# Optimization experiments

Measured on AMD Instinct MI355X. Metric: run time of the kernel, lower is better.

Reference implementation:

```python
import jax, jax.numpy as jnp
import numpy as np

IN_DIM = 256
QK_DIM = IN_DIM // 8


def setup_inputs() -> dict:
    key = jax.random.key(0)
    ks = jax.random.split(key, 10)
    B, C, W, H = 4, IN_DIM, 64, 64
    a = jax.random.normal(ks[0], (B, C, W, H), dtype=jnp.float32)
    b = jax.random.normal(ks[1], (B, C, W, H), dtype=jnp.float32)
    c = jax.random.uniform(ks[2], (B, 1, 2 * W, 2 * H), dtype=jnp.float32)
    scale = 0.02
    wq = jax.random.normal(ks[3], (QK_DIM, C), dtype=jnp.float32) * scale
    bq = jnp.zeros((QK_DIM,), dtype=jnp.float32)
    wk = jax.random.normal(ks[4], (QK_DIM, C), dtype=jnp.float32) * scale
    bk = jnp.zeros((QK_DIM,), dtype=jnp.float32)
    wv = jax.random.normal(ks[5], (C, C), dtype=jnp.float32) * scale
    bv = jnp.zeros((C,), dtype=jnp.float32)
    gamma = jnp.ones((1,), dtype=jnp.float32)
    return {"a": a, "b": b, "c": c, "wq": wq, "bq": bq, "wk": wk,
            "bk": bk, "wv": wv, "bv": bv, "gamma": gamma}


def reference(a, b, c, wq, bq, wk, bk, wv, bv, gamma):
    B, C, W, H = a.shape
    N = W * H
    # F.interpolate(c, scale_factor=1/down_rate, mode='nearest'): output idx i -> input idx i*down_rate
    down = c.shape[2] // W
    cd = c[:, :, ::down, ::down]                      # [B,1,W,H]
    # 1x1 convs as channel contractions
    q = jnp.einsum('bchw,oc->bohw', a, wq) + bq[None, :, None, None]
    k = jnp.einsum('bchw,oc->bohw', b, wk) + bk[None, :, None, None]
    v = jnp.einsum('bchw,oc->bohw', a, wv) + bv[None, :, None, None]
    qf = q.reshape(B, QK_DIM, N)                      # proj_query^T rows are spatial
    kf = k.reshape(B, QK_DIM, N)
    vf = v.reshape(B, C, N)
    sim = jnp.einsum('bdi,bdj->bij', qf, kf)          # [B,N,N]
    cflat = cd.reshape(B, N)
    # mask[b,i,j] = cflat[b,i] (per-query multiplicative logit scaling)
    logits = sim * cflat[:, :, None]
    attn = jax.nn.softmax(logits, axis=-1)            # [B,N,N]
    out_attn = jnp.einsum('bcj,bij->bci', vf, attn).reshape(B, C, W, H)
    out = gamma * a * cd + (1.0 - cd) * out_attn
    return out
```

## Files before the change

### kernel.cpp

```cpp
#include <hip/hip_runtime.h>

#define LOG2E 1.44269504088896340736f

typedef __attribute__((ext_vector_type(8))) short short8;
typedef __attribute__((ext_vector_type(4))) float float4v;
typedef __attribute__((ext_vector_type(2))) float float2v;
typedef __attribute__((ext_vector_type(2))) int int2v;
typedef __attribute__((ext_vector_type(4))) int int4v;

__device__ inline unsigned short f2bf(float f) {
    union { float f; unsigned u; } v; v.f = f;
    unsigned r = v.u + 0x7fffu + ((v.u >> 16) & 1u);
    return (unsigned short)(r >> 16);
}
__device__ inline float bf2f(unsigned short u) {
    union { unsigned u; float f; } v; v.u = ((unsigned)u) << 16;
    return v.f;
}
__device__ inline unsigned pk_bf16(float a, float b) {
    union { float f; unsigned u; } ua, ub; ua.f = a; ub.f = b;
    return __builtin_amdgcn_perm(ub.u + 0x8000u, ua.u + 0x8000u, 0x07060302u);
}

__global__ void wcvt_kernel(const float* __restrict__ wq, const float* __restrict__ wk,
                            const float* __restrict__ wv, unsigned short* __restrict__ Wbf)
{
    int idx = blockIdx.x * 256 + threadIdx.x;
    int e4  = idx * 4;
    int row = e4 >> 8, col = e4 & 255;
    const float* src = (row < 32) ? (wq + row * 256 + col)
                     : (row < 64) ? (wk + (row - 32) * 256 + col)
                                  : (wv + (row - 64) * 256 + col);
    float4v v = *(const float4v*)src;
    int2v p;
    p.x = (unsigned)f2bf(v[0]) | ((unsigned)f2bf(v[1]) << 16);
    p.y = (unsigned)f2bf(v[2]) | ((unsigned)f2bf(v[3]) << 16);
    *(int2v*)(Wbf + e4) = p;
}

__launch_bounds__(512, 2)
__global__ void proj_kernel(const float* __restrict__ a_p, const float* __restrict__ b_p,
                            const float* __restrict__ c_p,
                            const float* __restrict__ bq, const float* __restrict__ bk,
                            const float* __restrict__ bv,
                            const unsigned short* __restrict__ Wbf,
                            unsigned short* __restrict__ Qg, unsigned short* __restrict__ Kg,
                            unsigned short* __restrict__ Vg)
{
    __shared__ __align__(16) unsigned short At[64 * 264];
    __shared__ __align__(16) unsigned short Bt[64 * 264];
    __shared__ float bias[320];
    __shared__ float cdl[64];

    const int t    = threadIdx.x;
    const int blk  = blockIdx.x;
    const int b    = blk & 3;
    const int tile = blk >> 2;
    const int i0   = tile * 64;
    const int lane = t & 63;
    const int w    = t >> 6;
    const int q    = lane >> 4;
    const int n    = lane & 15;
    const int it   = w & 3;
    const int mh   = w >> 2;

    {
        const int arr = t >> 8, cp = (t >> 1) & 127, ih = (t & 1) * 32;
        const float* src = (arr ? b_p : a_p) + ((size_t)(b * 256 + 2 * cp)) * 4096 + i0 + ih;
        unsigned* dst = (unsigned*)(arr ? Bt : At) + cp;
#pragma unroll
        for (int h = 0; h < 4; ++h) {
            float4v r0a = *(const float4v*)(src + h * 8);
            float4v r0b = *(const float4v*)(src + h * 8 + 4);
            float4v r1a = *(const float4v*)(src + 4096 + h * 8);
            float4v r1b = *(const float4v*)(src + 4096 + h * 8 + 4);
#pragma unroll
            for (int jj = 0; jj < 4; ++jj)
                dst[(ih + h * 8 + jj) * 132] = pk_bf16(r0a[jj], r1a[jj]);
#pragma unroll
            for (int jj = 0; jj < 4; ++jj)
                dst[(ih + h * 8 + 4 + jj) * 132] = pk_bf16(r0b[jj], r1b[jj]);
        }
        if (t < 320) bias[t] = (t < 32) ? bq[t] : (t < 64) ? bk[t - 32] : bv[t - 64];
        else if (t < 384) cdl[t - 320] = c_p[b * 16384 + tile * 256 + (t - 320) * 2];
    }
    __syncthreads();

    float4v acc[10];
#pragma unroll
    for (int j = 0; j < 10; ++j) acc[j] = (float4v){0.f, 0.f, 0.f, 0.f};

#pragma unroll 2
    for (int kc = 0; kc < 8; ++kc) {
        short8 xa = *(const short8*)&At[(it * 16 + n) * 264 + kc * 32 + q * 8];
        short8 xb = xa;
        if (mh == 0)
            xb = *(const short8*)&Bt[(it * 16 + n) * 264 + kc * 32 + q * 8];
#pragma unroll
        for (int j = 0; j < 10; ++j) {
            int mt = mh * 10 + j;
            short8 wf = *(const short8*)(Wbf + (size_t)(mt * 16 + n) * 256 + kc * 32 + q * 8);
            short8 bsel = (mt == 2 || mt == 3) ? xb : xa;
            acc[j] = __builtin_amdgcn_mfma_f32_16x16x32_bf16(wf, bsel, acc[j], 0, 0, 0);
        }
    }
    __syncthreads();

    unsigned short* QKst = At;
    unsigned short* Vst  = Bt;
    {
        const float cdq = cdl[it * 16 + n] * LOG2E;
#pragma unroll
        for (int j = 0; j < 10; ++j) {
            int mt = mh * 10 + j;
            float4v bv4 = *(const float4v*)&bias[mt * 16 + q * 4];
            float v0 = acc[j][0] + bv4[0], v1 = acc[j][1] + bv4[1];
            float v2 = acc[j][2] + bv4[2], v3 = acc[j][3] + bv4[3];
            if (mt < 2) {
                v0 *= cdq; v1 *= cdq; v2 *= cdq; v3 *= cdq;
                int2v pk; pk.x = (int)pk_bf16(v0, v1); pk.y = (int)pk_bf16(v2, v3);
                *(int2v*)&QKst[(it * 16 + n) * 72 + mt * 16 + q * 4] = pk;
            } else if (mt < 4) {
                int2v pk; pk.x = (int)pk_bf16(v0, v1); pk.y = (int)pk_bf16(v2, v3);
                *(int2v*)&QKst[(it * 16 + n) * 72 + mt * 16 + q * 4] = pk;
            } else {
                int p = ((n >> 2) * 8) + ((it & 1) * 4) + (n & 3);
                int cbase = mt * 16 - 64 + q * 4;
                int jb = it >> 1;
                Vst[((jb * 256) + cbase + 0) * 32 + p] = f2bf(v0);
                Vst[((jb * 256) + cbase + 1) * 32 + p] = f2bf(v1);
                Vst[((jb * 256) + cbase + 2) * 32 + p] = f2bf(v2);
                Vst[((jb * 256) + cbase + 3) * 32 + p] = f2bf(v3);
            }
        }
    }
    __syncthreads();

    {
        int i = t >> 3, h8 = t & 7;
        int4v v = *(const int4v*)&QKst[i * 72 + h8 * 8];
        unsigned short* dstp = (h8 < 4)
            ? Qg + (size_t)(b * 4096 + i0 + i) * 32 + h8 * 8
            : Kg + (size_t)(b * 4096 + i0 + i) * 32 + (h8 - 4) * 8;
        *(int4v*)dstp = v;
    }
    {
#pragma unroll
        for (int k = 0; k < 4; ++k) {
            int flat = k * 512 + t;
            int4v v = *(const int4v*)&Vst[flat * 8];
            int jb = flat >> 10;
            *(int4v*)(Vg + (size_t)(b * 128 + tile * 2 + jb) * 8192 + (flat & 1023) * 8) = v;
        }
    }
}

__launch_bounds__(256, 3)
__global__ void attn_kernel(const unsigned short* __restrict__ Qg,
                            const unsigned short* __restrict__ Kg,
                            const unsigned short* __restrict__ Vg,
                            unsigned short* __restrict__ Opart, float* __restrict__ lsum)
{
    const int t    = threadIdx.x;
    const int blk  = blockIdx.x;
    const int b    = blk & 3;
    const int s_lo = (blk >> 2) & 1;
    const int rt   = (blk >> 3) & 63;
    const int s    = s_lo + 2 * (blk >> 9);
    const int lidx = (s << 8) | (rt << 2) | b;
    const int i0   = rt * 64;
    const int lane = t & 63;
    const int w    = t >> 6;
    const int q    = lane >> 4;
    const int n    = lane & 15;

    short8 qf[4];
#pragma unroll
    for (int ig = 0; ig < 4; ++ig)
        qf[ig] = *(const short8*)(Qg + (size_t)(b * 4096 + i0 + ig * 16 + n) * 32 + q * 8);

    float4v acc[4][4];
#pragma unroll
    for (int ig = 0; ig < 4; ++ig)
#pragma unroll
        for (int ct = 0; ct < 4; ++ct) acc[ig][ct] = (float4v){0.f, 0.f, 0.f, 0.f};
    float lsc[4] = {0.f, 0.f, 0.f, 0.f};

    const float4v m16v = (float4v){-16.f, -16.f, -16.f, -16.f};

    const unsigned short* kb = Kg + (size_t)(b * 4096 + s * 1024 + n) * 32 + q * 8;
    const unsigned short* vb = Vg + ((size_t)((b * 128 + s * 32) * 256 + w * 64 + n)) * 32 + q * 8;

    short8 kf0 = *(const short8*)(kb);
    short8 kf1 = *(const short8*)(kb + 512);

#pragma unroll 1
    for (int it = 0; it < 32; ++it) {
        short8 vf[4];
#pragma unroll
        for (int ct = 0; ct < 4; ++ct)
            vf[ct] = *(const short8*)(vb + ct * 512);

        short8 pf[4];
#pragma unroll
        for (int ig = 0; ig < 4; ++ig) {
            float4v s0 = __builtin_amdgcn_mfma_f32_16x16x32_bf16(kf0, qf[ig], m16v, 0, 0, 0);
            float4v s1 = __builtin_amdgcn_mfma_f32_16x16x32_bf16(kf1, qf[ig], m16v, 0, 0, 0);
            float p0 = __builtin_amdgcn_exp2f(s0[0]), p1 = __builtin_amdgcn_exp2f(s0[1]);
            float p2 = __builtin_amdgcn_exp2f(s0[2]), p3 = __builtin_amdgcn_exp2f(s0[3]);
            float p4 = __builtin_amdgcn_exp2f(s1[0]), p5 = __builtin_amdgcn_exp2f(s1[1]);
            float p6 = __builtin_amdgcn_exp2f(s1[2]), p7 = __builtin_amdgcn_exp2f(s1[3]);
            lsc[ig] += ((p0 + p1) + (p2 + p3)) + ((p4 + p5) + (p6 + p7));
            union { short8 s8; unsigned u[4]; } pf_;
            pf_.u[0] = pk_bf16(p0, p1);
            pf_.u[1] = pk_bf16(p2, p3);
            pf_.u[2] = pk_bf16(p4, p5);
            pf_.u[3] = pk_bf16(p6, p7);
            pf[ig] = pf_.s8;
        }

        kf0 = *(const short8*)(kb + 1024);
        kf1 = *(const short8*)(kb + 1536);

#pragma unroll
        for (int ig = 0; ig < 4; ++ig)
#pragma unroll
            for (int ct = 0; ct < 4; ++ct)
                acc[ig][ct] = __builtin_amdgcn_mfma_f32_16x16x32_bf16(pf[ig], vf[ct], acc[ig][ct], 0, 0, 0);

        kb += 1024;
        vb += 8192;
    }

    const size_t obase = (size_t)lidx * 16384;
#pragma unroll
    for (int ig = 0; ig < 4; ++ig)
#pragma unroll
        for (int ct = 0; ct < 4; ++ct) {
            int c = w * 64 + ct * 16 + n;
            int i = ig * 16 + q * 4;
            int2v pk;
            pk.x = (int)pk_bf16(acc[ig][ct][0], acc[ig][ct][1]);
            pk.y = (int)pk_bf16(acc[ig][ct][2], acc[ig][ct][3]);
            *(int2v*)(Opart + obase + (size_t)c * 64 + i) = pk;
        }
#pragma unroll
    for (int ig = 0; ig < 4; ++ig) {
        float v = lsc[ig];
        v += __shfl_xor(v, 16, 64);
        v += __shfl_xor(v, 32, 64);
        if (w == 0 && lane < 16)
            lsum[(size_t)lidx * 64 + ig * 16 + lane] = v;
    }
}

__launch_bounds__(256, 4)
__global__ void combine_kernel(const float* __restrict__ a_p, const float* __restrict__ c_p,
                               const float* __restrict__ gamma_p,
                               const unsigned short* __restrict__ Opart,
                               const float* __restrict__ lsum, float* __restrict__ out)
{
    __shared__ float invL[64];
    __shared__ float cdl[64];

    const int t   = threadIdx.x;
    const int blk = blockIdx.x;
    const int b   = blk & 3;
    const int rt  = (blk >> 2) & 63;
    const int cs  = blk >> 8;
    const int i0  = rt * 64;

    if (t < 64) {
        float L = 0.f;
#pragma unroll
        for (int s = 0; s < 4; ++s)
            L += lsum[(size_t)((s << 8) | (rt << 2) | b) * 64 + t];
        invL[t] = 1.0f / L;
        cdl[t] = c_p[b * 16384 + rt * 256 + 2 * t];
    }
    __syncthreads();

    const float gam = gamma_p[0];
    const int il = (t & 31) * 2;
    const int cq = t >> 5;
#pragma unroll
    for (int k = 0; k < 4; ++k) {
        int c = cs * 32 + cq + 8 * k;
        float o0 = 0.f, o1 = 0.f;
#pragma unroll
        for (int s = 0; s < 4; ++s) {
            int idx = (s << 8) | (rt << 2) | b;
            unsigned pr = *(const unsigned*)(Opart + (size_t)idx * 16384 + (size_t)c * 64 + il);
            o0 += bf2f((unsigned short)(pr & 0xffff));
            o1 += bf2f((unsigned short)(pr >> 16));
        }
        o0 *= invL[il];
        o1 *= invL[il + 1];
        size_t gi = (size_t)(b * 256 + c) * 4096 + i0 + il;
        float2v av = *(const float2v*)(a_p + gi);
        float cd0 = cdl[il], cd1 = cdl[il + 1];
        float2v ov;
        ov[0] = gam * av[0] * cd0 + (1.0f - cd0) * o0;
        ov[1] = gam * av[1] * cd1 + (1.0f - cd1) * o1;
        *(float2v*)(out + gi) = ov;
    }
}

extern "C" void kernel_launch(void* const* d_in, const int* in_sizes, int n_in,
                              void* d_out, int out_size, void* d_ws, size_t ws_size,
                              hipStream_t stream)
{
    const float* a_p   = (const float*)d_in[0];
    const float* b_p   = (const float*)d_in[1];
    const float* c_p   = (const float*)d_in[2];
    const float* wq    = (const float*)d_in[3];
    const float* bq    = (const float*)d_in[4];
    const float* wk    = (const float*)d_in[5];
    const float* bk    = (const float*)d_in[6];
    const float* wv    = (const float*)d_in[7];
    const float* bv    = (const float*)d_in[8];
    const float* gamma = (const float*)d_in[9];
    float* out = (float*)d_out;

    unsigned short* Qg    = (unsigned short*)d_ws;
    unsigned short* Kg    = Qg + (size_t)4 * 4096 * 32;
    unsigned short* Vg    = Kg + (size_t)4 * 4096 * 32;
    unsigned short* Wbf   = Vg + (size_t)4 * 256 * 4096;
    unsigned short* Opart = Wbf + (size_t)320 * 256;
    float*          lsum  = (float*)(Opart + (size_t)1024 * 16384);

    wcvt_kernel<<<80, 256, 0, stream>>>(wq, wk, wv, Wbf);
    proj_kernel<<<256, 512, 0, stream>>>(a_p, b_p, c_p, bq, bk, bv, Wbf, Qg, Kg, Vg);
    attn_kernel<<<1024, 256, 0, stream>>>(Qg, Kg, Vg, Opart, lsum);
    combine_kernel<<<2048, 256, 0, stream>>>(a_p, c_p, gamma, Opart, lsum, out);
}
```

Before: 188.4 us.

## Fuse weight bf16 conversion into projection, re-layout staging, add MFMA priority

Removes the separate weight-conversion kernel so the projection kernel reads fp32 weights and packs them to bf16 in registers right before each MFMA, saving one launch and a workspace round-trip. The activation staging loop is restructured so consecutive threads load consecutive pixels, and the LDS row stride is changed to 133 words to avoid bank conflicts. The attention kernel raises wave priority around the P·V MFMA block. The cost is that each of the 256 projection blocks now reads fp32 weights and converts them redundantly, which doubles weight load bytes and adds ALU work in the inner loop.

```diff
diff --git a/kernel.cpp b/kernel.cpp
--- a/kernel.cpp
+++ b/kernel.cpp
@@ -22,33 +22,18 @@
     return __builtin_amdgcn_perm(ub.u + 0x8000u, ua.u + 0x8000u, 0x07060302u);
 }
 
-__global__ void wcvt_kernel(const float* __restrict__ wq, const float* __restrict__ wk,
-                            const float* __restrict__ wv, unsigned short* __restrict__ Wbf)
-{
-    int idx = blockIdx.x * 256 + threadIdx.x;
-    int e4  = idx * 4;
-    int row = e4 >> 8, col = e4 & 255;
-    const float* src = (row < 32) ? (wq + row * 256 + col)
-                     : (row < 64) ? (wk + (row - 32) * 256 + col)
-                                  : (wv + (row - 64) * 256 + col);
-    float4v v = *(const float4v*)src;
-    int2v p;
-    p.x = (unsigned)f2bf(v[0]) | ((unsigned)f2bf(v[1]) << 16);
-    p.y = (unsigned)f2bf(v[2]) | ((unsigned)f2bf(v[3]) << 16);
-    *(int2v*)(Wbf + e4) = p;
-}
-
 __launch_bounds__(512, 2)
 __global__ void proj_kernel(const float* __restrict__ a_p, const float* __restrict__ b_p,
                             const float* __restrict__ c_p,
+                            const float* __restrict__ wq_p, const float* __restrict__ wk_p,
+                            const float* __restrict__ wv_p,
                             const float* __restrict__ bq, const float* __restrict__ bk,
                             const float* __restrict__ bv,
-                            const unsigned short* __restrict__ Wbf,
                             unsigned short* __restrict__ Qg, unsigned short* __restrict__ Kg,
                             unsigned short* __restrict__ Vg)
 {
-    __shared__ __align__(16) unsigned short At[64 * 264];
-    __shared__ __align__(16) unsigned short Bt[64 * 264];
+    __shared__ __align__(16) unsigned short At[64 * 266];
+    __shared__ __align__(16) unsigned short Bt[64 * 266];
     __shared__ float bias[320];
     __shared__ float cdl[64];
 
@@ -65,21 +50,19 @@
     const int mh   = w >> 2;
 
     {
-        const int arr = t >> 8, cp = (t >> 1) & 127, ih = (t & 1) * 32;
-        const float* src = (arr ? b_p : a_p) + ((size_t)(b * 256 + 2 * cp)) * 4096 + i0 + ih;
-        unsigned* dst = (unsigned*)(arr ? Bt : At) + cp;
-#pragma unroll
-        for (int h = 0; h < 4; ++h) {
-            float4v r0a = *(const float4v*)(src + h * 8);
-            float4v r0b = *(const float4v*)(src + h * 8 + 4);
-            float4v r1a = *(const float4v*)(src + 4096 + h * 8);
-            float4v r1b = *(const float4v*)(src + 4096 + h * 8 + 4);
-#pragma unroll
-            for (int jj = 0; jj < 4; ++jj)
-                dst[(ih + h * 8 + jj) * 132] = pk_bf16(r0a[jj], r1a[jj]);
-#pragma unroll
-            for (int jj = 0; jj < 4; ++jj)
-                dst[(ih + h * 8 + 4 + jj) * 132] = pk_bf16(r0b[jj], r1b[jj]);
+        const int arr = t >> 8, tt = t & 255;
+        unsigned* dst = (unsigned*)(arr ? Bt : At);
+        const float* base = (arr ? b_p : a_p) + (size_t)b * 256 * 4096 + i0;
+#pragma unroll
+        for (int r = 0; r < 8; ++r) {
+            int task = r * 256 + tt;
+            int cp = task >> 4, px4 = (task & 15) * 4;
+            const float* s0 = base + (size_t)(2 * cp) * 4096 + px4;
+            float4v r0 = *(const float4v*)s0;
+            float4v r1 = *(const float4v*)(s0 + 4096);
+#pragma unroll
+            for (int k = 0; k < 4; ++k)
+                dst[(px4 + k) * 133 + cp] = pk_bf16(r0[k], r1[k]);
         }
         if (t < 320) bias[t] = (t < 32) ? bq[t] : (t < 64) ? bk[t - 32] : bv[t - 64];
         else if (t < 384) cdl[t - 320] = c_p[b * 16384 + tile * 256 + (t - 320) * 2];
@@ -92,16 +75,26 @@
 
 #pragma unroll 2
     for (int kc = 0; kc < 8; ++kc) {
-        short8 xa = *(const short8*)&At[(it * 16 + n) * 264 + kc * 32 + q * 8];
+        short8 xa = *(const short8*)&At[(it * 16 + n) * 266 + kc * 32 + q * 8];
         short8 xb = xa;
         if (mh == 0)
-            xb = *(const short8*)&Bt[(it * 16 + n) * 264 + kc * 32 + q * 8];
+            xb = *(const short8*)&Bt[(it * 16 + n) * 266 + kc * 32 + q * 8];
 #pragma unroll
         for (int j = 0; j < 10; ++j) {
             int mt = mh * 10 + j;
-            short8 wf = *(const short8*)(Wbf + (size_t)(mt * 16 + n) * 256 + kc * 32 + q * 8);
+            const float* wbase = (mt < 2) ? wq_p : (mt < 4) ? wk_p : wv_p;
+            int mrow = (mt < 2) ? (mt * 16 + n) : (mt < 4) ? ((mt - 2) * 16 + n)
+                                                           : ((mt - 4) * 16 + n);
+            const float* wp = wbase + (size_t)mrow * 256 + kc * 32 + q * 8;
+            float4v wa = *(const float4v*)wp;
+            float4v wb2 = *(const float4v*)(wp + 4);
+            union { short8 s8; unsigned u[4]; } wf_;
+            wf_.u[0] = pk_bf16(wa[0], wa[1]);
+            wf_.u[1] = pk_bf16(wa[2], wa[3]);
+            wf_.u[2] = pk_bf16(wb2[0], wb2[1]);
+            wf_.u[3] = pk_bf16(wb2[2], wb2[3]);
             short8 bsel = (mt == 2 || mt == 3) ? xb : xa;
-            acc[j] = __builtin_amdgcn_mfma_f32_16x16x32_bf16(wf, bsel, acc[j], 0, 0, 0);
+            acc[j] = __builtin_amdgcn_mfma_f32_16x16x32_bf16(wf_.s8, bsel, acc[j], 0, 0, 0);
         }
     }
     __syncthreads();
@@ -222,11 +215,13 @@
         kf0 = *(const short8*)(kb + 1024);
         kf1 = *(const short8*)(kb + 1536);
 
+        __builtin_amdgcn_s_setprio(1);
 #pragma unroll
         for (int ig = 0; ig < 4; ++ig)
 #pragma unroll
             for (int ct = 0; ct < 4; ++ct)
                 acc[ig][ct] = __builtin_amdgcn_mfma_f32_16x16x32_bf16(pf[ig], vf[ct], acc[ig][ct], 0, 0, 0);
+        __builtin_amdgcn_s_setprio(0);
 
         kb += 1024;
         vb += 8192;
@@ -325,12 +320,10 @@
     unsigned short* Qg    = (unsigned short*)d_ws;
     unsigned short* Kg    = Qg + (size_t)4 * 4096 * 32;
     unsigned short* Vg    = Kg + (size_t)4 * 4096 * 32;
-    unsigned short* Wbf   = Vg + (size_t)4 * 256 * 4096;
-    unsigned short* Opart = Wbf + (size_t)320 * 256;
+    unsigned short* Opart = Vg + (size_t)4 * 256 * 4096;
     float*          lsum  = (float*)(Opart + (size_t)1024 * 16384);
 
-    wcvt_kernel<<<80, 256, 0, stream>>>(wq, wk, wv, Wbf);
-    proj_kernel<<<256, 512, 0, stream>>>(a_p, b_p, c_p, bq, bk, bv, Wbf, Qg, Kg, Vg);
+    proj_kernel<<<256, 512, 0, stream>>>(a_p, b_p, c_p, wq, wk, wv, bq, bk, bv, Qg, Kg, Vg);
     attn_kernel<<<1024, 256, 0, stream>>>(Qg, Kg, Vg, Opart, lsum);
     combine_kernel<<<2048, 256, 0, stream>>>(a_p, c_p, gamma, Opart, lsum, out);
 }
```

New measurement: 197.5 us. 1.05x slower.

## Compute softmax row sums via MFMA with ones, use hardware bf16 pack, retune proj staging

Applied to the files above, without the earlier changes.

In the attention kernel, the per-row exponential sums move from scalar VALU adds to an extra MFMA against a ones vector, which also removes the final cross-lane shuffles. The P packing switches from the perm-based rounding trick to the v_cvt_pk_bf16_f32 instruction, and the MFMA block is wrapped in s_setprio. In the projection kernel, the input transpose-to-LDS staging is reorganised so each thread loads contiguous pixels, and the LDS row pitch changes to 266 (133 words) to reduce bank conflicts. Together these cut VALU work in the hot loop at the cost of one extra MFMA per query group per iteration. The sums now come from bf16-rounded P, which matches the values fed to the PV MFMAs but adds rounding.

```diff
diff --git a/kernel.cpp b/kernel.cpp
--- a/kernel.cpp
+++ b/kernel.cpp
@@ -20,6 +20,11 @@
 __device__ inline unsigned pk_bf16(float a, float b) {
     union { float f; unsigned u; } ua, ub; ua.f = a; ub.f = b;
     return __builtin_amdgcn_perm(ub.u + 0x8000u, ua.u + 0x8000u, 0x07060302u);
+}
+__device__ inline unsigned cvtpk_bf16(float a, float b) {
+    unsigned r;
+    asm("v_cvt_pk_bf16_f32 %0, %1, %2" : "=v"(r) : "v"(a), "v"(b));
+    return r;
 }
 
 __global__ void wcvt_kernel(const float* __restrict__ wq, const float* __restrict__ wk,
@@ -47,8 +52,8 @@
                             unsigned short* __restrict__ Qg, unsigned short* __restrict__ Kg,
                             unsigned short* __restrict__ Vg)
 {
-    __shared__ __align__(16) unsigned short At[64 * 264];
-    __shared__ __align__(16) unsigned short Bt[64 * 264];
+    __shared__ __align__(16) unsigned short At[64 * 266];
+    __shared__ __align__(16) unsigned short Bt[64 * 266];
     __shared__ float bias[320];
     __shared__ float cdl[64];
 
@@ -65,21 +70,19 @@
     const int mh   = w >> 2;
 
     {
-        const int arr = t >> 8, cp = (t >> 1) & 127, ih = (t & 1) * 32;
-        const float* src = (arr ? b_p : a_p) + ((size_t)(b * 256 + 2 * cp)) * 4096 + i0 + ih;
-        unsigned* dst = (unsigned*)(arr ? Bt : At) + cp;
-#pragma unroll
-        for (int h = 0; h < 4; ++h) {
-            float4v r0a = *(const float4v*)(src + h * 8);
-            float4v r0b = *(const float4v*)(src + h * 8 + 4);
-            float4v r1a = *(const float4v*)(src + 4096 + h * 8);
-            float4v r1b = *(const float4v*)(src + 4096 + h * 8 + 4);
-#pragma unroll
-            for (int jj = 0; jj < 4; ++jj)
-                dst[(ih + h * 8 + jj) * 132] = pk_bf16(r0a[jj], r1a[jj]);
-#pragma unroll
-            for (int jj = 0; jj < 4; ++jj)
-                dst[(ih + h * 8 + 4 + jj) * 132] = pk_bf16(r0b[jj], r1b[jj]);
+        const int arr = t >> 8, tt = t & 255;
+        unsigned* dst = (unsigned*)(arr ? Bt : At);
+        const float* base = (arr ? b_p : a_p) + (size_t)b * 256 * 4096 + i0;
+#pragma unroll
+        for (int r = 0; r < 8; ++r) {
+            int task = r * 256 + tt;
+            int cp = task >> 4, px4 = (task & 15) * 4;
+            const float* s0 = base + (size_t)(2 * cp) * 4096 + px4;
+            float4v r0 = *(const float4v*)s0;
+            float4v r1 = *(const float4v*)(s0 + 4096);
+#pragma unroll
+            for (int k = 0; k < 4; ++k)
+                dst[(px4 + k) * 133 + cp] = pk_bf16(r0[k], r1[k]);
         }
         if (t < 320) bias[t] = (t < 32) ? bq[t] : (t < 64) ? bk[t - 32] : bv[t - 64];
         else if (t < 384) cdl[t - 320] = c_p[b * 16384 + tile * 256 + (t - 320) * 2];
@@ -92,10 +95,10 @@
 
 #pragma unroll 2
     for (int kc = 0; kc < 8; ++kc) {
-        short8 xa = *(const short8*)&At[(it * 16 + n) * 264 + kc * 32 + q * 8];
+        short8 xa = *(const short8*)&At[(it * 16 + n) * 266 + kc * 32 + q * 8];
         short8 xb = xa;
         if (mh == 0)
-            xb = *(const short8*)&Bt[(it * 16 + n) * 264 + kc * 32 + q * 8];
+            xb = *(const short8*)&Bt[(it * 16 + n) * 266 + kc * 32 + q * 8];
 #pragma unroll
         for (int j = 0; j < 10; ++j) {
             int mt = mh * 10 + j;
@@ -174,17 +177,23 @@
     const int q    = lane >> 4;
     const int n    = lane & 15;
 
+    union { short8 s8; unsigned u[4]; } ones_;
+    ones_.u[0] = ones_.u[1] = ones_.u[2] = ones_.u[3] = 0x3F803F80u;
+    const short8 ones8 = ones_.s8;
+
     short8 qf[4];
 #pragma unroll
     for (int ig = 0; ig < 4; ++ig)
         qf[ig] = *(const short8*)(Qg + (size_t)(b * 4096 + i0 + ig * 16 + n) * 32 + q * 8);
 
     float4v acc[4][4];
-#pragma unroll
-    for (int ig = 0; ig < 4; ++ig)
+    float4v lacc[4];
+#pragma unroll
+    for (int ig = 0; ig < 4; ++ig) {
+        lacc[ig] = (float4v){0.f, 0.f, 0.f, 0.f};
 #pragma unroll
         for (int ct = 0; ct < 4; ++ct) acc[ig][ct] = (float4v){0.f, 0.f, 0.f, 0.f};
-    float lsc[4] = {0.f, 0.f, 0.f, 0.f};
+    }
 
     const float4v m16v = (float4v){-16.f, -16.f, -16.f, -16.f};
 
@@ -210,23 +219,26 @@
             float p2 = __builtin_amdgcn_exp2f(s0[2]), p3 = __builtin_amdgcn_exp2f(s0[3]);
             float p4 = __builtin_amdgcn_exp2f(s1[0]), p5 = __builtin_amdgcn_exp2f(s1[1]);
             float p6 = __builtin_amdgcn_exp2f(s1[2]), p7 = __builtin_amdgcn_exp2f(s1[3]);
-            lsc[ig] += ((p0 + p1) + (p2 + p3)) + ((p4 + p5) + (p6 + p7));
             union { short8 s8; unsigned u[4]; } pf_;
-            pf_.u[0] = pk_bf16(p0, p1);
-            pf_.u[1] = pk_bf16(p2, p3);
-            pf_.u[2] = pk_bf16(p4, p5);
-            pf_.u[3] = pk_bf16(p6, p7);
+            pf_.u[0] = cvtpk_bf16(p0, p1);
+            pf_.u[1] = cvtpk_bf16(p2, p3);
+            pf_.u[2] = cvtpk_bf16(p4, p5);
+            pf_.u[3] = cvtpk_bf16(p6, p7);
             pf[ig] = pf_.s8;
         }
 
         kf0 = *(const short8*)(kb + 1024);
         kf1 = *(const short8*)(kb + 1536);
 
-#pragma unroll
-        for (int ig = 0; ig < 4; ++ig)
+        __builtin_amdgcn_s_setprio(1);
+#pragma unroll
+        for (int ig = 0; ig < 4; ++ig) {
+            lacc[ig] = __builtin_amdgcn_mfma_f32_16x16x32_bf16(pf[ig], ones8, lacc[ig], 0, 0, 0);
 #pragma unroll
             for (int ct = 0; ct < 4; ++ct)
                 acc[ig][ct] = __builtin_amdgcn_mfma_f32_16x16x32_bf16(pf[ig], vf[ct], acc[ig][ct], 0, 0, 0);
+        }
+        __builtin_amdgcn_s_setprio(0);
 
         kb += 1024;
         vb += 8192;
@@ -244,13 +256,12 @@
             pk.y = (int)pk_bf16(acc[ig][ct][2], acc[ig][ct][3]);
             *(int2v*)(Opart + obase + (size_t)c * 64 + i) = pk;
         }
-#pragma unroll
-    for (int ig = 0; ig < 4; ++ig) {
-        float v = lsc[ig];
-        v += __shfl_xor(v, 16, 64);
-        v += __shfl_xor(v, 32, 64);
-        if (w == 0 && lane < 16)
-            lsum[(size_t)lidx * 64 + ig * 16 + lane] = v;
+    if (w == 0 && n == 0) {
+#pragma unroll
+        for (int ig = 0; ig < 4; ++ig)
+#pragma unroll
+            for (int r = 0; r < 4; ++r)
+                lsum[(size_t)lidx * 64 + ig * 16 + q * 4 + r] = lacc[ig][r];
     }
 }
 
```

Result: faster. 182.2 us (-3.3%).
